# Kernel tuning notes

Measured on AMD Instinct MI355X. Metric: run time of the kernel, lower is better.

The kernel has to match this reference:

```python
import jax, jax.numpy as jnp
import numpy as np

B, M, H, D, C = 512, 40, 128, 64, 128


def setup_inputs() -> dict:
    key = jax.random.key(0)
    k1, k2, k3, k4 = jax.random.split(key, 4)
    x0 = jax.random.normal(k1, (B, M, D), dtype=jnp.float32)
    xk = jax.random.normal(k2, (B, H, D), dtype=jnp.float32)
    # Conv1d(kernel_size=1) weight [C, H*M, 1] squeezed to [C, H*M]; bias [C]
    W = jax.random.normal(k3, (C, H * M), dtype=jnp.float32) * 0.02
    b = jax.random.normal(k4, (C,), dtype=jnp.float32) * 0.02
    return {"x0": x0, "xk": xk, "W": W, "b": b}


def reference(x0, xk, W, b):
    # torch: outer[b, h*M+m, d] = xk[b,h,d] * x0[b,m,d]; out = conv1d(outer)
    # conv1d with kernel_size=1 is a channel contraction:
    #   out[b,c,d] = sum_{h,m} W[c, h*M+m] * xk[b,h,d] * x0[b,m,d] + b[c]
    Bsz, Hh, Dd = xk.shape
    Mm = x0.shape[1]
    Cc = W.shape[0]
    Wr = W.reshape(Cc, Hh, Mm)  # channel index is h*M + m -> [C, H, M]
    out = jnp.einsum('bhd,bmd,chm->bcd', xk, x0, Wr) + b[None, :, None]
    return out  # [B, C, D]
```

## Files before the change

### kernel.cpp

```cpp
#include <hip/hip_runtime.h>
#include <hip/hip_bf16.h>

typedef __attribute__((ext_vector_type(8))) short short8;
typedef __attribute__((ext_vector_type(4))) float f32x4;
typedef unsigned short u16;
typedef unsigned int u32;

#define NB 512
#define NM 40
#define NH 128
#define ND 64
#define NC 128
#define KTOT 5120

__device__ __forceinline__ u16 f2bf_rne(float f) {
    u32 u = __float_as_uint(f);
    u32 r = u + 0x7FFFu + ((u >> 16) & 1u);
    return (u16)(r >> 16);
}

__global__ void w3_kernel(const float* __restrict__ W, u16* __restrict__ W3) {
    __shared__ u16 kbuf[KTOT];
    const int c = blockIdx.x;
    const float* src = W + (size_t)c * KTOT;
    for (int k = threadIdx.x; k < KTOT; k += 256)
        kbuf[k] = f2bf_rne(src[k]);
    __syncthreads();
    for (int n = threadIdx.x; n < 640; n += 256) {
        int m = n >> 4, t = (n >> 2) & 3, q = n & 3;
        union { short8 s8; u16 e[8]; } v;
#pragma unroll
        for (int j = 0; j < 8; ++j)
            v.e[j] = kbuf[(t * 32 + q * 8 + j) * NM + m];
        *(short8*)(W3 + ((size_t)n * 128 + c) * 8) = v.s8;
    }
}

__global__ void __launch_bounds__(512, 2) cin_main(
    const float* __restrict__ x0g, const float* __restrict__ xkg,
    const float* __restrict__ biasg, const u16* __restrict__ W3,
    float* __restrict__ out)
{
    __shared__ __align__(16) char smem[70144];
    short* xkT    = (short*)smem;
    float* x0s    = (float*)(smem + 34816);
    float* red    = (float*)smem;
    float* bias_s = (float*)(smem + 69632);

    const int tid = threadIdx.x;
    const int w = tid >> 6, L = tid & 63;
    const int q = L >> 4, l16 = L & 15;
    const int bh = (w >> 2) & 1;
    const int rh = (w >> 1) & 1;
    const int mh = w & 1;
    const size_t b0 = 2 * (size_t)blockIdx.x;

    const u16* Ap = W3 + q * 1024 + (size_t)(rh * 64 + l16) * 8;
    const int m0 = mh * 20;

    short8 aP[2][4];
    auto loadAstep = [&](int u, short8* dst) {
        const size_t m = (size_t)(m0 + (u >> 2));
        const int t = u & 3;
        const u16* p = Ap + m * 16384 + t * 4096;
#pragma unroll
        for (int mt = 0; mt < 4; ++mt)
            dst[mt] = *(const short8*)(p + mt * 128);
    };
    loadAstep(0, aP[0]);
    loadAstep(1, aP[1]);

    {
        for (int i = tid; i < 4096; i += 512) {
            int bn = i >> 11, rem = i & 2047;
            int h = rem >> 4, d4 = (rem & 15) << 2;
            float4 v = *(const float4*)(xkg + (b0 + bn) * (NH * ND) + h * ND + d4);
            short* xT = xkT + bn * 8704;
            xT[(d4 + 0) * 136 + h] = (short)f2bf_rne(v.x);
            xT[(d4 + 1) * 136 + h] = (short)f2bf_rne(v.y);
            xT[(d4 + 2) * 136 + h] = (short)f2bf_rne(v.z);
            xT[(d4 + 3) * 136 + h] = (short)f2bf_rne(v.w);
        }
        for (int i = tid; i < 1280; i += 512) {
            int bn = i / 640, rem = i % 640;
            int m = rem >> 4, d4 = (rem & 15) << 2;
            *(f32x4*)(x0s + bn * 2720 + m * 68 + d4) =
                *(const f32x4*)(x0g + (b0 + bn) * (NM * ND) + m * ND + d4);
        }
        if (tid < NC) bias_s[tid] = biasg[tid];
    }
    __syncthreads();

    const short* xT = xkT + bh * 8704;
    const float* x0p = x0s + bh * 2720;
    const short* Bp = xT + (size_t)l16 * 136 + q * 8;
    short8 bR[4][4];
#pragma unroll
    for (int t = 0; t < 4; ++t)
#pragma unroll
        for (int n = 0; n < 4; ++n)
            bR[t][n] = *(const short8*)(Bp + n * (16 * 136) + t * 32);

    float s[4], sn[4];
#pragma unroll
    for (int n = 0; n < 4; ++n)
        s[n] = x0p[m0 * 68 + n * 16 + l16];

    f32x4 T[4][4] = {};
    f32x4 o[4][4] = {};

#pragma unroll 4
    for (int u = 0; u < 80; ++u) {
        const int t = u & 3;
        short8* aC = aP[u & 1];
        if (t == 0) {
            const int m = m0 + (u >> 2);
#pragma unroll
            for (int n = 0; n < 4; ++n)
                sn[n] = ((u >> 2) < 19) ? x0p[(m + 1) * 68 + n * 16 + l16] : 0.f;
        }
#pragma unroll
        for (int n = 0; n < 4; ++n) {
            T[0][n] = __builtin_amdgcn_mfma_f32_16x16x32_bf16(aC[0], bR[t][n], T[0][n], 0, 0, 0);
            T[1][n] = __builtin_amdgcn_mfma_f32_16x16x32_bf16(aC[1], bR[t][n], T[1][n], 0, 0, 0);
            T[2][n] = __builtin_amdgcn_mfma_f32_16x16x32_bf16(aC[2], bR[t][n], T[2][n], 0, 0, 0);
            T[3][n] = __builtin_amdgcn_mfma_f32_16x16x32_bf16(aC[3], bR[t][n], T[3][n], 0, 0, 0);
        }
        const int up = (u + 2 < 80) ? (u + 2) : u;
        loadAstep(up, aC);
        if (t == 3) {
#pragma unroll
            for (int n = 0; n < 4; ++n) {
                const float dd = s[n] - sn[n];
#pragma unroll
                for (int mt = 0; mt < 4; ++mt)
                    o[mt][n] += dd * T[mt][n];
                s[n] = sn[n];
            }
        }
    }

    __syncthreads();
    float* myred = red + (bh * 2 + rh) * 4352;
    if (mh == 1) {
#pragma unroll
        for (int mt = 0; mt < 4; ++mt)
#pragma unroll
            for (int n = 0; n < 4; ++n) {
                int d = n * 16 + l16;
                *(f32x4*)(myred + d * 68 + mt * 16 + q * 4) = o[mt][n];
            }
    }
    __syncthreads();
    if (mh == 0) {
        float* op = out + (b0 + bh) * (NC * ND);
#pragma unroll
        for (int mt = 0; mt < 4; ++mt)
#pragma unroll
            for (int n = 0; n < 4; ++n) {
                int d = n * 16 + l16;
                f32x4 r = *(const f32x4*)(myred + d * 68 + mt * 16 + q * 4);
#pragma unroll
                for (int rr = 0; rr < 4; ++rr) {
                    int c = rh * 64 + mt * 16 + q * 4 + rr;
                    op[c * ND + d] = o[mt][n][rr] + r[rr] + bias_s[c];
                }
            }
    }
}

extern "C" void kernel_launch(void* const* d_in, const int* in_sizes, int n_in,
                              void* d_out, int out_size, void* d_ws, size_t ws_size,
                              hipStream_t stream) {
    const float* x0 = (const float*)d_in[0];
    const float* xk = (const float*)d_in[1];
    const float* W  = (const float*)d_in[2];
    const float* bi = (const float*)d_in[3];
    float* out = (float*)d_out;

    u16* W3 = (u16*)d_ws;

    w3_kernel<<<NC, 256, 0, stream>>>(W, W3);
    cin_main<<<NB / 2, 512, 0, stream>>>(x0, xk, bi, W3, out);
}
```

Measured before the change: 117.3 us.

## Deepen W prefetch, stream xk B-fragments from LDS, split weight prep

After: 114.5 us. -2.5%, faster.

```diff
diff --git a/kernel.cpp b/kernel.cpp
--- a/kernel.cpp
+++ b/kernel.cpp
@@ -20,18 +20,24 @@
 }
 
 __global__ void w3_kernel(const float* __restrict__ W, u16* __restrict__ W3) {
-    __shared__ u16 kbuf[KTOT];
-    const int c = blockIdx.x;
-    const float* src = W + (size_t)c * KTOT;
-    for (int k = threadIdx.x; k < KTOT; k += 256)
-        kbuf[k] = f2bf_rne(src[k]);
-    __syncthreads();
-    for (int n = threadIdx.x; n < 640; n += 256) {
-        int m = n >> 4, t = (n >> 2) & 3, q = n & 3;
+    __shared__ u16 kbuf[NH * 20];
+    const int c = blockIdx.x >> 1, mh = blockIdx.x & 1;
+    const float* src = W + (size_t)c * KTOT + mh * 20;
+    for (int i = threadIdx.x; i < NH * 5; i += 256) {
+        int h = i / 5, j4 = i % 5;
+        float4 v = *(const float4*)(src + h * NM + j4 * 4);
+        u16* kb = kbuf + h * 20 + j4 * 4;
+        kb[0] = f2bf_rne(v.x); kb[1] = f2bf_rne(v.y);
+        kb[2] = f2bf_rne(v.z); kb[3] = f2bf_rne(v.w);
+    }
+    __syncthreads();
+    for (int i = threadIdx.x; i < 320; i += 256) {
+        int mo = i >> 4, t = (i >> 2) & 3, q = i & 3;
+        int n = (mh * 20 + mo) * 16 + t * 4 + q;
         union { short8 s8; u16 e[8]; } v;
 #pragma unroll
         for (int j = 0; j < 8; ++j)
-            v.e[j] = kbuf[(t * 32 + q * 8 + j) * NM + m];
+            v.e[j] = kbuf[(t * 32 + q * 8 + j) * 20 + mo];
         *(short8*)(W3 + ((size_t)n * 128 + c) * 8) = v.s8;
     }
 }
@@ -58,17 +64,19 @@
     const u16* Ap = W3 + q * 1024 + (size_t)(rh * 64 + l16) * 8;
     const int m0 = mh * 20;
 
-    short8 aP[2][4];
-    auto loadAstep = [&](int u, short8* dst) {
-        const size_t m = (size_t)(m0 + (u >> 2));
-        const int t = u & 3;
-        const u16* p = Ap + m * 16384 + t * 4096;
+    short8 aP[4][4];
+    auto loadAstep = [&](int u2, short8* dst) {
+        const size_t m = (size_t)(m0 + (u2 >> 2));
+        const int tt = u2 & 3;
+        const u16* p = Ap + m * 16384 + tt * 4096;
 #pragma unroll
         for (int mt = 0; mt < 4; ++mt)
             dst[mt] = *(const short8*)(p + mt * 128);
     };
     loadAstep(0, aP[0]);
     loadAstep(1, aP[1]);
+    loadAstep(2, aP[2]);
+    loadAstep(3, aP[3]);
 
     {
         for (int i = tid; i < 4096; i += 512) {
@@ -91,15 +99,17 @@
     }
     __syncthreads();
 
-    const short* xT = xkT + bh * 8704;
     const float* x0p = x0s + bh * 2720;
-    const short* Bp = xT + (size_t)l16 * 136 + q * 8;
-    short8 bR[4][4];
-#pragma unroll
-    for (int t = 0; t < 4; ++t)
+    int bofs = bh * 17408 + l16 * 272 + q * 16;
+
+    short8 bB[2][4];
+    auto loadB = [&](int tt, short8* dst, int bo) {
+        const char* bsrc = (const char*)xkT + bo + tt * 64;
 #pragma unroll
         for (int n = 0; n < 4; ++n)
-            bR[t][n] = *(const short8*)(Bp + n * (16 * 136) + t * 32);
+            dst[n] = *(const short8*)(bsrc + n * 4352);
+    };
+    loadB(0, bB[0], bofs);
 
     float s[4], sn[4];
 #pragma unroll
@@ -109,25 +119,28 @@
     f32x4 T[4][4] = {};
     f32x4 o[4][4] = {};
 
-#pragma unroll 4
-    for (int u = 0; u < 80; ++u) {
+    auto body = [&](int u, bool lastB) {
         const int t = u & 3;
-        short8* aC = aP[u & 1];
+        short8* aC = aP[u & 3];
+        const short8* bC = bB[u & 1];
+        if (!lastB) {
+            asm volatile("" : "+v"(bofs));
+            loadB((u + 1) & 3, bB[(u + 1) & 1], bofs);
+        }
         if (t == 0) {
             const int m = m0 + (u >> 2);
 #pragma unroll
             for (int n = 0; n < 4; ++n)
-                sn[n] = ((u >> 2) < 19) ? x0p[(m + 1) * 68 + n * 16 + l16] : 0.f;
+                sn[n] = (m < m0 + 19) ? x0p[(m + 1) * 68 + n * 16 + l16] : 0.f;
         }
 #pragma unroll
         for (int n = 0; n < 4; ++n) {
-            T[0][n] = __builtin_amdgcn_mfma_f32_16x16x32_bf16(aC[0], bR[t][n], T[0][n], 0, 0, 0);
-            T[1][n] = __builtin_amdgcn_mfma_f32_16x16x32_bf16(aC[1], bR[t][n], T[1][n], 0, 0, 0);
-            T[2][n] = __builtin_amdgcn_mfma_f32_16x16x32_bf16(aC[2], bR[t][n], T[2][n], 0, 0, 0);
-            T[3][n] = __builtin_amdgcn_mfma_f32_16x16x32_bf16(aC[3], bR[t][n], T[3][n], 0, 0, 0);
-        }
-        const int up = (u + 2 < 80) ? (u + 2) : u;
-        loadAstep(up, aC);
+            T[0][n] = __builtin_amdgcn_mfma_f32_16x16x32_bf16(aC[0], bC[n], T[0][n], 0, 0, 0);
+            T[1][n] = __builtin_amdgcn_mfma_f32_16x16x32_bf16(aC[1], bC[n], T[1][n], 0, 0, 0);
+            T[2][n] = __builtin_amdgcn_mfma_f32_16x16x32_bf16(aC[2], bC[n], T[2][n], 0, 0, 0);
+            T[3][n] = __builtin_amdgcn_mfma_f32_16x16x32_bf16(aC[3], bC[n], T[3][n], 0, 0, 0);
+        }
+        if (u < 76) loadAstep(u + 4, aC);
         if (t == 3) {
 #pragma unroll
             for (int n = 0; n < 4; ++n) {
@@ -138,7 +151,14 @@
                 s[n] = sn[n];
             }
         }
-    }
+    };
+
+#pragma unroll 4
+    for (int u = 0; u < 76; ++u)
+        body(u, false);
+#pragma unroll
+    for (int u = 76; u < 80; ++u)
+        body(u, u == 79);
 
     __syncthreads();
     float* myred = red + (bh * 2 + rh) * 4352;
@@ -180,6 +200,6 @@
 
     u16* W3 = (u16*)d_ws;
 
-    w3_kernel<<<NC, 256, 0, stream>>>(W, W3);
+    w3_kernel<<<NC * 2, 256, 0, stream>>>(W, W3);
     cin_main<<<NB / 2, 512, 0, stream>>>(x0, xk, bi, W3, out);
 }
```
